# Performance work log

Hardware: AMD Instinct MI355X
Metric: run time of the kernel (lower is better)

The kernel has to match this reference:

```python
import jax, jax.numpy as jnp
import numpy as np

B, D_IN, HID = 8192, 1024, 2048
H_PH, DELTA0 = 64, 7.0
N_EXP, EXP_DIM = 16, 128
VOCAB, N_CLS = 32000, 1000
K_WIN, DECAY, THETA = 20, 0.8, 1.2
N_TOK = 100
ENH = HID + 2 * H_PH  # retrieval-core input dim


def setup_inputs() -> dict:
    key = jax.random.key(0)
    ks = jax.random.split(key, 16)
    s = lambda d: 1.0 / np.sqrt(d)
    return {
        "x": jax.random.normal(ks[0], (B, D_IN), jnp.float32),
        "W_in": jax.random.normal(ks[1], (D_IN, HID), jnp.float32) * s(D_IN),
        "b_in": jnp.zeros((HID,), jnp.float32),
        "Wg": jax.random.normal(ks[2], (ENH, N_EXP), jnp.float32) * s(ENH),
        "bg": jnp.zeros((N_EXP,), jnp.float32),
        "We": jax.random.normal(ks[3], (N_EXP, ENH, EXP_DIM), jnp.float32) * s(ENH),
        "be": jnp.zeros((N_EXP, EXP_DIM), jnp.float32),
        "Wo": jax.random.normal(ks[4], (EXP_DIM, HID), jnp.float32) * s(EXP_DIM),
        "bo": jnp.zeros((HID,), jnp.float32),
        "Wh": jax.random.normal(ks[5], (3, HID, HID), jnp.float32) * s(HID),
        "bh": jnp.zeros((3, HID), jnp.float32),
        "Wcls": jax.random.normal(ks[6], (HID, N_CLS), jnp.float32) * s(HID),
        "bcls": jnp.zeros((N_CLS,), jnp.float32),
    }


def reference(x, W_in, b_in, Wg, bg, We, be, Wo, bo, Wh, bh, Wcls, bcls):
    # input projection
    proj = x @ W_in + b_in                                  # [B, HID]
    # phasor bank on per-sample mean (vmapped oscillator bank)
    t = jnp.mean(proj, axis=-1)                             # [B]
    harm = jnp.arange(1, H_PH + 1, dtype=proj.dtype)        # [H]
    phase = DELTA0 * t[:, None] * harm[None, :]             # [B, H]
    temporal = jnp.concatenate([jnp.sin(phase), jnp.cos(phase)], axis=-1)  # [B, 2H]
    enh = jnp.concatenate([proj, temporal], axis=-1)        # [B, ENH]
    # 16-expert retrieval core: softmax gate, relu experts, dense readout
    gate = jax.nn.softmax(enh @ Wg + bg, axis=-1)           # [B, E]
    expert = jax.nn.relu(jnp.einsum('bd,edk->bek', enh, We) + be)  # [B, E, K]
    combined = jnp.einsum('be,bek->bk', gate, expert)       # [B, K]
    context = combined @ Wo + bo                            # [B, HID]
    # spiking top-k attention over modulo-indexed tokens from sample 0
    tok = jnp.argsort(jnp.abs(context[0]))[-N_TOK:] % VOCAB  # [100] int

    def step(v, ti):
        v = DECAY * v
        v = v.at[ti].add(1.0)
        spk = v > THETA
        return jnp.where(spk, 0.0, v), spk.astype(context.dtype)

    _, spikes = jax.lax.scan(step, jnp.zeros((VOCAB,), context.dtype), tok)
    counts = spikes.sum(axis=0)                             # [VOCAB]
    _, top_idx = jax.lax.top_k(counts, K_WIN)
    gains = jnp.ones((VOCAB,), context.dtype).at[top_idx].add(1.0)
    attended = context * gains[: context.shape[-1]]         # [B, HID]
    # trailing dense MLP
    h = attended
    for i in range(3):
        h = jax.nn.relu(h @ Wh[i] + bh[i])
    return h @ Wcls + bcls                                  # [B, N_CLS]
```

## Files before the change

kernel.cpp:

```cpp
#include <hip/hip_runtime.h>
#include <math.h>


typedef unsigned short u16;
typedef __attribute__((ext_vector_type(8))) short bfrag8;
typedef __attribute__((ext_vector_type(4))) float facc4;

__device__ __forceinline__ u16 f2bf(float f) {
  union { float f; unsigned u; } c; c.f = f;
  unsigned u = c.u;
  return (u16)((u + 0x7fffu + ((u >> 16) & 1u)) >> 16);
}
__device__ __forceinline__ float bf2f(u16 h) {
  union { unsigned u; float f; } c; c.u = ((unsigned)h) << 16;
  return c.f;
}
__device__ __forceinline__ void gload16(const void* g, void* lds) {
  __builtin_amdgcn_global_load_lds(
      (const __attribute__((address_space(1))) unsigned*)g,
      (__attribute__((address_space(3))) unsigned*)lds, 16, 0, 0);
}

#define BARX() do { __builtin_amdgcn_sched_barrier(0); \
  __builtin_amdgcn_s_barrier(); __builtin_amdgcn_sched_barrier(0); } while (0)
#define LGKM0() do { asm volatile("s_waitcnt lgkmcnt(0)" ::: "memory"); \
  __builtin_amdgcn_sched_barrier(0); } while (0)
#define VMWN() do { if constexpr (MFR == 8) \
    asm volatile("s_waitcnt vmcnt(4)" ::: "memory"); \
  else asm volatile("s_waitcnt vmcnt(2)" ::: "memory"); \
  __builtin_amdgcn_sched_barrier(0); } while (0)

#define RDA_(dst, mbase, dbuf) do { \
  char* _b = smem + (dbuf) * DBUF; \
  _Pragma("unroll") for (int mm = 0; mm < MFRH; ++mm) { \
    int _row = wr * (BM / 2) + ((mbase) + mm) * 16 + r15; \
    _Pragma("unroll") for (int ks = 0; ks < 2; ++ks) \
      dst[mm][ks] = *(const bfrag8*)(_b + _row * 128 + \
                                     (((g + ks * 4) ^ (_row & 7)) << 4)); \
  } } while (0)

#define RDB_(dst, nbase, dbuf) do { \
  char* _b = smem + (dbuf) * DBUF + AREG; \
  _Pragma("unroll") for (int nn = 0; nn < 2; ++nn) { \
    int _row = wc * 64 + ((nbase) + nn) * 16 + r15; \
    _Pragma("unroll") for (int ks = 0; ks < 2; ++ks) \
      dst[nn][ks] = *(const bfrag8*)(_b + _row * 128 + \
                                     (((g + ks * 4) ^ (_row & 7)) << 4)); \
  } } while (0)

#define MF_(a, b, mo, no) do { \
  __builtin_amdgcn_s_setprio(1); \
  _Pragma("unroll") for (int mm = 0; mm < MFRH; ++mm) \
  _Pragma("unroll") for (int nn = 0; nn < 2; ++nn) \
  _Pragma("unroll") for (int ks = 0; ks < 2; ++ks) \
    acc[(mo) + mm][(no) + nn] = __builtin_amdgcn_mfma_f32_16x16x32_bf16( \
        a[mm][ks], b[nn][ks], acc[(mo) + mm][(no) + nn], 0, 0, 0); \
  __builtin_amdgcn_s_setprio(0); \
} while (0)

enum { EP_PROJ = 0, EP_EXPERT = 1, EP_CTX = 2, EP_RELU = 3, EP_OUT = 4 };

template<int EP, int MFR>
__global__ __launch_bounds__(512, 2)
void gemm8(const u16* __restrict__ A, const u16* __restrict__ Bt,
           const float* __restrict__ bias, void* __restrict__ Cp,
           const float* __restrict__ gate, float* __restrict__ partials,
           int K, int lda, int ldb, int ldc, int nvalid)
{
  constexpr int MFRH = MFR / 2;
  constexpr int BM = MFR * 32;
  constexpr int AHALF = MFR * 2048;
  constexpr int AREG = MFR * 4096;
  constexpr int DBUF = AREG + 32768;

  extern __shared__ char smem[];
  const int t = threadIdx.x;
  const int lane = t & 63, wid = t >> 6;
  const int wr = wid >> 2, wc = wid & 3;
  const int g = lane >> 4, r15 = lane & 15;

  const int nblk = gridDim.x * gridDim.y;
  const int flat = blockIdx.y * gridDim.x + blockIdx.x;
  const int swz = (flat & 7) * (nblk >> 3) + (flat >> 3);
  const int bx = swz % gridDim.x, by = swz / gridDim.x;

  const long a0 = (long)(by * BM) * lda;
  const long b0 = (long)(bx * 256) * ldb;

  facc4 acc[MFR][4];
#pragma unroll
  for (int m = 0; m < MFR; m++)
#pragma unroll
    for (int n = 0; n < 4; n++) acc[m][n] = (facc4){0.f, 0.f, 0.f, 0.f};

  const int r0 = t >> 3, c0s = t & 7;
  const int csw = ((c0s ^ (r0 & 7)) << 3);

  auto STAGE = [&](int kt, int which, int dbuf) {
    const int half = which & 1;
    if (which < 2) {
      char* ldst = smem + dbuf * DBUF + half * AHALF;
      const u16* gsrc =
          A + a0 + (long)(half * (BM / 2) + r0) * lda + kt * 64 + csw;
      gload16(gsrc, ldst + (t << 4));
      if (MFR == 8) gload16(gsrc + 64L * lda, ldst + ((512 + t) << 4));
    } else {
      char* ldst = smem + dbuf * DBUF + AREG + half * 16384;
      const u16* gsrc =
          Bt + b0 + (long)(half * 128 + r0) * ldb + kt * 64 + csw;
      gload16(gsrc, ldst + (t << 4));
      gload16(gsrc + 64L * ldb, ldst + ((512 + t) << 4));
    }
  };

  const int NT = K >> 6;
  STAGE(0, 0, 0); STAGE(0, 1, 0); STAGE(0, 2, 0); STAGE(0, 3, 0);
  STAGE(1, 0, 1); STAGE(1, 1, 1);
  VMWN(); BARX();

  bfrag8 aE[MFRH][2], aO[MFRH][2], b01[2][2], b23[2][2];

  for (int it = 0; it < (NT >> 1); ++it) {
    const int T = 2 * it;
    const int tp1 = T + 1;
    const int tp2 = (T + 2 < NT) ? T + 2 : NT - 1;
    const int tp3 = (T + 3 < NT) ? T + 3 : NT - 1;
    RDA_(aE, 0, 0); RDB_(b01, 0, 0); STAGE(tp1, 2, 1);
    LGKM0(); MF_(aE, b01, 0, 0); BARX();
    RDA_(aO, MFRH, 0); STAGE(tp1, 3, 1);
    LGKM0(); MF_(aO, b01, MFRH, 0); BARX();
    RDB_(b23, 2, 0); STAGE(tp2, 0, 0); STAGE(tp2, 1, 0);
    LGKM0(); MF_(aO, b23, MFRH, 2); MF_(aE, b23, 0, 2);
    VMWN(); BARX();
    RDA_(aE, 0, 1); RDB_(b01, 0, 1); STAGE(tp2, 2, 0);
    LGKM0(); MF_(aE, b01, 0, 0); BARX();
    RDA_(aO, MFRH, 1); STAGE(tp2, 3, 0);
    LGKM0(); MF_(aO, b01, MFRH, 0); BARX();
    RDB_(b23, 2, 1); STAGE(tp3, 0, 1); STAGE(tp3, 1, 1);
    LGKM0(); MF_(aO, b23, MFRH, 2); MF_(aE, b23, 0, 2);
    VMWN(); BARX();
  }

  asm volatile("s_waitcnt vmcnt(0)" ::: "memory");
  __builtin_amdgcn_sched_barrier(0);
  __builtin_amdgcn_s_barrier();
  __builtin_amdgcn_sched_barrier(0);

  const int rbase = by * BM + wr * (BM / 2);
  const int cbase = bx * 256 + wc * 64;
  float* slab = (float*)(smem + wid * 8704);

  float psum[MFR][4];
  if (EP == EP_PROJ) {
#pragma unroll
    for (int m = 0; m < MFR; m++)
#pragma unroll
      for (int r = 0; r < 4; r++) psum[m][r] = 0.f;
  }

#pragma unroll
  for (int pass = 0; pass < MFRH; ++pass) {
#pragma unroll
    for (int mm = 0; mm < 2; ++mm) {
      const int m = pass * 2 + mm;
#pragma unroll
      for (int n = 0; n < 4; ++n)
#pragma unroll
        for (int r = 0; r < 4; ++r) {
          const int rowp = mm * 16 + g * 4 + r;
          const int grow = rbase + m * 16 + g * 4 + r;
          const int gcol = cbase + n * 16 + r15;
          float val = acc[m][n][r] + bias[gcol];
          if (EP == EP_EXPERT)
            val = fmaxf(val, 0.f) * gate[(long)grow * 16 + (gcol >> 7)];
          if (EP == EP_CTX && gcol < 20) val *= 2.0f;
          if (EP == EP_RELU) val = fmaxf(val, 0.f);
          if (EP == EP_PROJ) psum[m][r] += val;
          slab[rowp * 68 + n * 16 + r15] = val;
        }
    }
#pragma unroll
    for (int rep = 0; rep < 4; ++rep) {
      const int rowp = rep * 8 + (lane >> 3);
      const int cc = (lane & 7) * 8;
      const facc4 v0 = *(const facc4*)&slab[rowp * 68 + cc];
      const facc4 v1 = *(const facc4*)&slab[rowp * 68 + cc + 4];
      const long grow = rbase + pass * 32 + rowp;
      const int gcol0 = cbase + cc;
      if (EP == EP_OUT) {
        float* Cf = (float*)Cp;
        if (gcol0 + 7 < nvalid) {
          *(facc4*)(Cf + grow * ldc + gcol0) = v0;
          *(facc4*)(Cf + grow * ldc + gcol0 + 4) = v1;
        } else {
#pragma unroll
          for (int j = 0; j < 4; ++j)
            if (gcol0 + j < nvalid) Cf[grow * ldc + gcol0 + j] = v0[j];
#pragma unroll
          for (int j = 0; j < 4; ++j)
            if (gcol0 + 4 + j < nvalid) Cf[grow * ldc + gcol0 + 4 + j] = v1[j];
        }
      } else {
        u16 o[8];
        o[0] = f2bf(v0[0]); o[1] = f2bf(v0[1]);
        o[2] = f2bf(v0[2]); o[3] = f2bf(v0[3]);
        o[4] = f2bf(v1[0]); o[5] = f2bf(v1[1]);
        o[6] = f2bf(v1[2]); o[7] = f2bf(v1[3]);
        *(uint4*)((u16*)Cp + grow * ldc + gcol0) = *(const uint4*)o;
      }
    }
  }

  if (EP == EP_PROJ) {
#pragma unroll
    for (int m = 0; m < MFR; m++)
#pragma unroll
      for (int r = 0; r < 4; r++) {
        float p = psum[m][r];
        p += __shfl_xor(p, 1); p += __shfl_xor(p, 2);
        p += __shfl_xor(p, 4); p += __shfl_xor(p, 8);
        if (r15 == 0)
          partials[(long)(rbase + m * 16 + g * 4 + r) * 32 + bx * 4 + wc] = p;
      }
  }
}

__global__ __launch_bounds__(256)
void transpose_conv_k(const float* __restrict__ in, u16* __restrict__ out,
                      int K, int N, int ldout, long in_zstride, int out_zrows)
{
  __shared__ float tile[64][65];
  const int t = threadIdx.x;
  const int n0 = blockIdx.x * 64, k0 = blockIdx.y * 64;
  const float* src = in + (long)blockIdx.z * in_zstride;
  const int rr = t >> 4;
  const int cc = (t & 15) * 4;
#pragma unroll
  for (int j = 0; j < 4; j++) {
    int k = k0 + j * 16 + rr;
    int n = n0 + cc;
    float v0 = 0.f, v1 = 0.f, v2 = 0.f, v3 = 0.f;
    if (n + 3 < N) {
      facc4 v = *(const facc4*)(src + (long)k * N + n);
      v0 = v[0]; v1 = v[1]; v2 = v[2]; v3 = v[3];
    } else {
      if (n < N)     v0 = src[(long)k * N + n];
      if (n + 1 < N) v1 = src[(long)k * N + n + 1];
      if (n + 2 < N) v2 = src[(long)k * N + n + 2];
      if (n + 3 < N) v3 = src[(long)k * N + n + 3];
    }
    float* trow = &tile[j * 16 + rr][cc];
    trow[0] = v0; trow[1] = v1; trow[2] = v2; trow[3] = v3;
  }
  __syncthreads();
  const int n_l = t >> 2;
  const int kc = (t & 3) * 16;
  const int n_gl = n0 + n_l;
  u16 o16[16];
  const bool valid = n_gl < N;
#pragma unroll
  for (int i = 0; i < 16; i++) o16[i] = valid ? f2bf(tile[kc + i][n_l]) : (u16)0;
  long orow = (long)blockIdx.z * out_zrows + n_gl;
  u16* dst = out + orow * (long)ldout + k0 + kc;
  *(uint4*)dst = ((const uint4*)o16)[0];
  *(uint4*)(dst + 8) = ((const uint4*)o16)[1];
}

__global__ __launch_bounds__(256)
void f32_to_bf16_k(const float* __restrict__ in, u16* __restrict__ out)
{
  const long i = ((long)blockIdx.x * 256 + threadIdx.x) * 8;
  facc4 v0 = *(const facc4*)(in + i);
  facc4 v1 = *(const facc4*)(in + i + 4);
  u16 o[8];
  o[0] = f2bf(v0[0]); o[1] = f2bf(v0[1]); o[2] = f2bf(v0[2]); o[3] = f2bf(v0[3]);
  o[4] = f2bf(v1[0]); o[5] = f2bf(v1[1]); o[6] = f2bf(v1[2]); o[7] = f2bf(v1[3]);
  *(uint4*)(out + i) = *(const uint4*)o;
}

__global__ __launch_bounds__(128)
void temporal_k(const float* __restrict__ partials, u16* __restrict__ enh)
{
  __shared__ float tsh;
  const int b = blockIdx.x;
  const int j = threadIdx.x;
  if (j < 32) {
    float p = partials[(long)b * 32 + j];
    p += __shfl_xor(p, 1); p += __shfl_xor(p, 2); p += __shfl_xor(p, 4);
    p += __shfl_xor(p, 8); p += __shfl_xor(p, 16);
    if (j == 0) tsh = p;
  }
  __syncthreads();
  float tmean = tsh * (1.0f / 2048.0f);
  float v;
  if (j < 64) v = sinf(7.0f * tmean * (float)(j + 1));
  else        v = cosf(7.0f * tmean * (float)(j - 63));
  enh[(long)b * 2176 + 2048 + j] = f2bf(v);
}

__global__ __launch_bounds__(64)
void gate2_k(const u16* __restrict__ enh, const u16* __restrict__ Wgt,
             const float* __restrict__ bg, float* __restrict__ gate)
{
  const int lane = threadIdx.x & 63;
  const int g = lane >> 4, r15 = lane & 15;
  const long rowbase = (long)blockIdx.x * 16;

  const u16* arow = enh + (rowbase + r15) * 2176 + g * 8;
  const u16* brow = Wgt + (long)r15 * 2176 + g * 8;

  facc4 acc = (facc4){0.f, 0.f, 0.f, 0.f};
#pragma unroll 4
  for (int kt = 0; kt < 2176; kt += 64) {
    bfrag8 a0 = *(const bfrag8*)(arow + kt);
    bfrag8 b0 = *(const bfrag8*)(brow + kt);
    bfrag8 a1 = *(const bfrag8*)(arow + kt + 32);
    bfrag8 b1 = *(const bfrag8*)(brow + kt + 32);
    acc = __builtin_amdgcn_mfma_f32_16x16x32_bf16(a0, b0, acc, 0, 0, 0);
    acc = __builtin_amdgcn_mfma_f32_16x16x32_bf16(a1, b1, acc, 0, 0, 0);
  }

  const float bb = bg[r15];
#pragma unroll
  for (int r = 0; r < 4; ++r) {
    float v = acc[r] + bb;
    float mx = v;
    mx = fmaxf(mx, __shfl_xor(mx, 1)); mx = fmaxf(mx, __shfl_xor(mx, 2));
    mx = fmaxf(mx, __shfl_xor(mx, 4)); mx = fmaxf(mx, __shfl_xor(mx, 8));
    float ex = expf(v - mx);
    float sum = ex;
    sum += __shfl_xor(sum, 1); sum += __shfl_xor(sum, 2);
    sum += __shfl_xor(sum, 4); sum += __shfl_xor(sum, 8);
    gate[(rowbase + g * 4 + r) * 16 + r15] = ex / sum;
  }
}

__global__ __launch_bounds__(256)
void combine_k(const u16* __restrict__ expw, u16* __restrict__ comb)
{
  const long i = ((long)blockIdx.x * 256 + threadIdx.x) * 8;
  const long b = i >> 7;
  const int k = (int)(i & 127);
  float s[8] = {0.f, 0.f, 0.f, 0.f, 0.f, 0.f, 0.f, 0.f};
#pragma unroll
  for (int e = 0; e < 16; ++e) {
    uint4 v = *(const uint4*)(expw + b * 2048 + e * 128 + k);
    const u16* vp = (const u16*)&v;
#pragma unroll
    for (int j = 0; j < 8; ++j) s[j] += bf2f(vp[j]);
  }
  u16 o[8];
#pragma unroll
  for (int j = 0; j < 8; ++j) o[j] = f2bf(s[j]);
  *(uint4*)(comb + i) = *(const uint4*)o;
}

extern "C" void kernel_launch(void* const* d_in, const int* in_sizes, int n_in,
                              void* d_out, int out_size, void* d_ws,
                              size_t ws_size, hipStream_t stream)
{
  const float* x    = (const float*)d_in[0];
  const float* W_in = (const float*)d_in[1];
  const float* b_in = (const float*)d_in[2];
  const float* Wg   = (const float*)d_in[3];
  const float* bg   = (const float*)d_in[4];
  const float* We   = (const float*)d_in[5];
  const float* be   = (const float*)d_in[6];
  const float* Wo   = (const float*)d_in[7];
  const float* bo   = (const float*)d_in[8];
  const float* Wh   = (const float*)d_in[9];
  const float* bh   = (const float*)d_in[10];
  const float* Wcls = (const float*)d_in[11];
  const float* bcls = (const float*)d_in[12];
  float* out = (float*)d_out;

  char* ws = (char*)d_ws;
  u16* enhb   = (u16*)(ws);
  u16* bufF   = (u16*)(ws + 35651584);
  u16* bufA   = (u16*)(ws + 69206016);
  u16* Wt_o   = (u16*)(ws + 78118912);
  u16* bufW1  = (u16*)(ws + 78643200);
  u16* bufW2  = (u16*)(ws + 87031808);
  u16* comb   = (u16*)(ws + 95420416);
  float* partials = (float*)(ws + 97517568);
  float* gate     = (float*)(ws + 98566144);
  u16* Wt_in  = bufF;
  u16* xb     = bufF + 2097152;
  u16* Wgt    = bufF;
  u16* Wt_e   = bufA;
  u16* Wt_cls = bufA;

  hipFuncSetAttribute((const void*)gemm8<EP_PROJ, 8>,
                      hipFuncAttributeMaxDynamicSharedMemorySize, 131072);
  hipFuncSetAttribute((const void*)gemm8<EP_EXPERT, 8>,
                      hipFuncAttributeMaxDynamicSharedMemorySize, 131072);
  hipFuncSetAttribute((const void*)gemm8<EP_CTX, 8>,
                      hipFuncAttributeMaxDynamicSharedMemorySize, 131072);
  hipFuncSetAttribute((const void*)gemm8<EP_RELU, 8>,
                      hipFuncAttributeMaxDynamicSharedMemorySize, 131072);
  hipFuncSetAttribute((const void*)gemm8<EP_OUT, 4>,
                      hipFuncAttributeMaxDynamicSharedMemorySize, 98304);

  f32_to_bf16_k<<<4096, 256, 0, stream>>>(x, xb);
  transpose_conv_k<<<dim3(32, 16, 1), 256, 0, stream>>>(W_in, Wt_in, 1024, 2048, 1024, 0, 0);
  transpose_conv_k<<<dim3(2, 34, 16), 256, 0, stream>>>(We, Wt_e, 2176, 128, 2176, 2176L * 128L, 128);
  transpose_conv_k<<<dim3(32, 2, 1), 256, 0, stream>>>(Wo, Wt_o, 128, 2048, 128, 0, 0);
  transpose_conv_k<<<dim3(32, 32, 2), 256, 0, stream>>>(Wh, bufW1, 2048, 2048, 2048, 2048L * 2048L, 2048);

  gemm8<EP_PROJ, 8><<<dim3(8, 32), 512, 131072, stream>>>(
      xb, Wt_in, b_in, (void*)enhb, nullptr, partials, 1024, 1024, 1024, 2176, 2048);
  temporal_k<<<8192, 128, 0, stream>>>(partials, enhb);
  transpose_conv_k<<<dim3(1, 34, 1), 256, 0, stream>>>(Wg, Wgt, 2176, 16, 2176, 0, 0);
  gate2_k<<<512, 64, 0, stream>>>(enhb, Wgt, bg, gate);
  gemm8<EP_EXPERT, 8><<<dim3(8, 32), 512, 131072, stream>>>(
      enhb, Wt_e, be, (void*)bufF, gate, nullptr, 2176, 2176, 2176, 2048, 2048);
  transpose_conv_k<<<dim3(16, 32, 1), 256, 0, stream>>>(Wcls, Wt_cls, 2048, 1000, 2048, 0, 0);
  combine_k<<<512, 256, 0, stream>>>(bufF, comb);
  gemm8<EP_CTX, 8><<<dim3(8, 32), 512, 131072, stream>>>(
      comb, Wt_o, bo, (void*)enhb, nullptr, nullptr, 128, 128, 128, 2048, 2048);
  gemm8<EP_RELU, 8><<<dim3(8, 32), 512, 131072, stream>>>(
      enhb, bufW1, bh, (void*)bufF, nullptr, nullptr, 2048, 2048, 2048, 2048, 2048);
  transpose_conv_k<<<dim3(32, 32, 1), 256, 0, stream>>>(Wh + 2L * 2048L * 2048L, bufW1, 2048, 2048, 2048, 0, 0);
  gemm8<EP_RELU, 8><<<dim3(8, 32), 512, 131072, stream>>>(
      bufF, bufW2, bh + 2048, (void*)enhb, nullptr, nullptr, 2048, 2048, 2048, 2048, 2048);
  gemm8<EP_RELU, 8><<<dim3(8, 32), 512, 131072, stream>>>(
      enhb, bufW1, bh + 4096, (void*)bufF, nullptr, nullptr, 2048, 2048, 2048, 2048, 2048);
  gemm8<EP_OUT, 4><<<dim3(4, 64), 512, 98304, stream>>>(
      bufF, Wt_cls, bcls, (void*)out, nullptr, nullptr, 2048, 2048, 2048, 1000, 1000);
}
```

Measured before the change: 377.1 us.

## Switch GEMM inner loop to 32x32x16 MFMA with blocked LDS layout

Replaces the 16x16x32 bf16 MFMA tiles with 32x32x16 MFMA instructions. The LDS staging layout changes from an XOR-swizzled row layout to a blocked layout of 32-row by 8-k chunks, so each lane reads contiguous 16-byte fragments without swizzle math. The epilogue is rewritten for the 16-register accumulator layout, and the projection row-sum reduction moves inside each pass. The aim is fewer MFMA issues and LDS reads per FLOP. The risks are bank conflicts in the unswizzled layout and higher register pressure from the larger accumulators.

```diff
diff --git a/kernel.cpp b/kernel.cpp
--- a/kernel.cpp
+++ b/kernel.cpp
@@ -5,6 +5,7 @@
 typedef unsigned short u16;
 typedef __attribute__((ext_vector_type(8))) short bfrag8;
 typedef __attribute__((ext_vector_type(4))) float facc4;
+typedef __attribute__((ext_vector_type(16))) float facc16;
 
 __device__ __forceinline__ u16 f2bf(float f) {
   union { float f; unsigned u; } c; c.f = f;
@@ -30,31 +31,27 @@
   else asm volatile("s_waitcnt vmcnt(2)" ::: "memory"); \
   __builtin_amdgcn_sched_barrier(0); } while (0)
 
-#define RDA_(dst, mbase, dbuf) do { \
+#define RDA32(dst, mbase, dbuf) do { \
   char* _b = smem + (dbuf) * DBUF; \
-  _Pragma("unroll") for (int mm = 0; mm < MFRH; ++mm) { \
-    int _row = wr * (BM / 2) + ((mbase) + mm) * 16 + r15; \
-    _Pragma("unroll") for (int ks = 0; ks < 2; ++ks) \
-      dst[mm][ks] = *(const bfrag8*)(_b + _row * 128 + \
-                                     (((g + ks * 4) ^ (_row & 7)) << 4)); \
+  _Pragma("unroll") for (int mm = 0; mm < HB; ++mm) { \
+    char* _s = _b + (wr * MBW + (mbase) + mm) * 4096 + l31 * 16 + lh * 512; \
+    _Pragma("unroll") for (int kb = 0; kb < 4; ++kb) \
+      dst[mm][kb] = *(const bfrag8*)(_s + kb * 1024); \
   } } while (0)
 
-#define RDB_(dst, nbase, dbuf) do { \
-  char* _b = smem + (dbuf) * DBUF + AREG; \
-  _Pragma("unroll") for (int nn = 0; nn < 2; ++nn) { \
-    int _row = wc * 64 + ((nbase) + nn) * 16 + r15; \
-    _Pragma("unroll") for (int ks = 0; ks < 2; ++ks) \
-      dst[nn][ks] = *(const bfrag8*)(_b + _row * 128 + \
-                                     (((g + ks * 4) ^ (_row & 7)) << 4)); \
-  } } while (0)
-
-#define MF_(a, b, mo, no) do { \
+#define RDB32(dst, bnh, dbuf) do { \
+  char* _s = smem + (dbuf) * DBUF + AREG + (bnh) * 16384 + wc * 4096 + \
+             l31 * 16 + lh * 512; \
+  _Pragma("unroll") for (int kb = 0; kb < 4; ++kb) \
+    dst[kb] = *(const bfrag8*)(_s + kb * 1024); \
+} while (0)
+
+#define MF32(a, b, mo, nb) do { \
   __builtin_amdgcn_s_setprio(1); \
-  _Pragma("unroll") for (int mm = 0; mm < MFRH; ++mm) \
-  _Pragma("unroll") for (int nn = 0; nn < 2; ++nn) \
-  _Pragma("unroll") for (int ks = 0; ks < 2; ++ks) \
-    acc[(mo) + mm][(no) + nn] = __builtin_amdgcn_mfma_f32_16x16x32_bf16( \
-        a[mm][ks], b[nn][ks], acc[(mo) + mm][(no) + nn], 0, 0, 0); \
+  _Pragma("unroll") for (int kb = 0; kb < 4; ++kb) \
+  _Pragma("unroll") for (int mm = 0; mm < HB; ++mm) \
+    acc[(mo) + mm][nb] = __builtin_amdgcn_mfma_f32_32x32x16_bf16( \
+        a[mm][kb], b[kb], acc[(mo) + mm][nb], 0, 0, 0); \
   __builtin_amdgcn_s_setprio(0); \
 } while (0)
 
@@ -67,7 +64,8 @@
            const float* __restrict__ gate, float* __restrict__ partials,
            int K, int lda, int ldb, int ldc, int nvalid)
 {
-  constexpr int MFRH = MFR / 2;
+  constexpr int MBW = MFR / 2;
+  constexpr int HB = MBW / 2;
   constexpr int BM = MFR * 32;
   constexpr int AHALF = MFR * 2048;
   constexpr int AREG = MFR * 4096;
@@ -77,7 +75,7 @@
   const int t = threadIdx.x;
   const int lane = t & 63, wid = t >> 6;
   const int wr = wid >> 2, wc = wid & 3;
-  const int g = lane >> 4, r15 = lane & 15;
+  const int l31 = lane & 31, lh = lane >> 5;
 
   const int nblk = gridDim.x * gridDim.y;
   const int flat = blockIdx.y * gridDim.x + blockIdx.x;
@@ -87,29 +85,47 @@
   const long a0 = (long)(by * BM) * lda;
   const long b0 = (long)(bx * 256) * ldb;
 
-  facc4 acc[MFR][4];
-#pragma unroll
-  for (int m = 0; m < MFR; m++)
-#pragma unroll
-    for (int n = 0; n < 4; n++) acc[m][n] = (facc4){0.f, 0.f, 0.f, 0.f};
-
-  const int r0 = t >> 3, c0s = t & 7;
-  const int csw = ((c0s ^ (r0 & 7)) << 3);
+  facc16 acc[MBW][2];
+#pragma unroll
+  for (int m = 0; m < MBW; m++)
+#pragma unroll
+    for (int n = 0; n < 2; n++)
+#pragma unroll
+      for (int i = 0; i < 16; i++) acc[m][n][i] = 0.f;
+
+  const int s_kc = (t >> 5) & 7;
+  const int s_r = t & 31;
 
   auto STAGE = [&](int kt, int which, int dbuf) {
     const int half = which & 1;
     if (which < 2) {
       char* ldst = smem + dbuf * DBUF + half * AHALF;
-      const u16* gsrc =
-          A + a0 + (long)(half * (BM / 2) + r0) * lda + kt * 64 + csw;
-      gload16(gsrc, ldst + (t << 4));
-      if (MFR == 8) gload16(gsrc + 64L * lda, ldst + ((512 + t) << 4));
+      {
+        const int mb = t >> 8;
+        const u16* gsrc = A + a0 +
+            (long)(half * (BM / 2) + mb * 32 + s_r) * lda + kt * 64 + s_kc * 8;
+        gload16(gsrc, ldst + (t << 4));
+      }
+      if (MFR == 8) {
+        const int mb = 2 + (t >> 8);
+        const u16* gsrc = A + a0 +
+            (long)(half * (BM / 2) + mb * 32 + s_r) * lda + kt * 64 + s_kc * 8;
+        gload16(gsrc, ldst + ((512 + t) << 4));
+      }
     } else {
       char* ldst = smem + dbuf * DBUF + AREG + half * 16384;
-      const u16* gsrc =
-          Bt + b0 + (long)(half * 128 + r0) * ldb + kt * 64 + csw;
-      gload16(gsrc, ldst + (t << 4));
-      gload16(gsrc + 64L * ldb, ldst + ((512 + t) << 4));
+      {
+        const int s = t >> 8;
+        const u16* gsrc = Bt + b0 +
+            (long)(s * 64 + half * 32 + s_r) * ldb + kt * 64 + s_kc * 8;
+        gload16(gsrc, ldst + (t << 4));
+      }
+      {
+        const int s = 2 + (t >> 8);
+        const u16* gsrc = Bt + b0 +
+            (long)(s * 64 + half * 32 + s_r) * ldb + kt * 64 + s_kc * 8;
+        gload16(gsrc, ldst + ((512 + t) << 4));
+      }
     }
   };
 
@@ -118,26 +134,26 @@
   STAGE(1, 0, 1); STAGE(1, 1, 1);
   VMWN(); BARX();
 
-  bfrag8 aE[MFRH][2], aO[MFRH][2], b01[2][2], b23[2][2];
+  bfrag8 aE[HB][4], aO[HB][4], bn0[4], bn1[4];
 
   for (int it = 0; it < (NT >> 1); ++it) {
     const int T = 2 * it;
     const int tp1 = T + 1;
     const int tp2 = (T + 2 < NT) ? T + 2 : NT - 1;
     const int tp3 = (T + 3 < NT) ? T + 3 : NT - 1;
-    RDA_(aE, 0, 0); RDB_(b01, 0, 0); STAGE(tp1, 2, 1);
-    LGKM0(); MF_(aE, b01, 0, 0); BARX();
-    RDA_(aO, MFRH, 0); STAGE(tp1, 3, 1);
-    LGKM0(); MF_(aO, b01, MFRH, 0); BARX();
-    RDB_(b23, 2, 0); STAGE(tp2, 0, 0); STAGE(tp2, 1, 0);
-    LGKM0(); MF_(aO, b23, MFRH, 2); MF_(aE, b23, 0, 2);
+    RDA32(aE, 0, 0); RDB32(bn0, 0, 0); STAGE(tp1, 2, 1);
+    LGKM0(); MF32(aE, bn0, 0, 0); BARX();
+    RDA32(aO, HB, 0); STAGE(tp1, 3, 1);
+    LGKM0(); MF32(aO, bn0, HB, 0); BARX();
+    RDB32(bn1, 1, 0); STAGE(tp2, 0, 0); STAGE(tp2, 1, 0);
+    LGKM0(); MF32(aO, bn1, HB, 1); MF32(aE, bn1, 0, 1);
     VMWN(); BARX();
-    RDA_(aE, 0, 1); RDB_(b01, 0, 1); STAGE(tp2, 2, 0);
-    LGKM0(); MF_(aE, b01, 0, 0); BARX();
-    RDA_(aO, MFRH, 1); STAGE(tp2, 3, 0);
-    LGKM0(); MF_(aO, b01, MFRH, 0); BARX();
-    RDB_(b23, 2, 1); STAGE(tp3, 0, 1); STAGE(tp3, 1, 1);
-    LGKM0(); MF_(aO, b23, MFRH, 2); MF_(aE, b23, 0, 2);
+    RDA32(aE, 0, 1); RDB32(bn0, 0, 1); STAGE(tp2, 2, 0);
+    LGKM0(); MF32(aE, bn0, 0, 0); BARX();
+    RDA32(aO, HB, 1); STAGE(tp2, 3, 0);
+    LGKM0(); MF32(aO, bn0, HB, 0); BARX();
+    RDB32(bn1, 1, 1); STAGE(tp3, 0, 1); STAGE(tp3, 1, 1);
+    LGKM0(); MF32(aO, bn1, HB, 1); MF32(aE, bn1, 0, 1);
     VMWN(); BARX();
   }
 
@@ -150,34 +166,44 @@
   const int cbase = bx * 256 + wc * 64;
   float* slab = (float*)(smem + wid * 8704);
 
-  float psum[MFR][4];
-  if (EP == EP_PROJ) {
-#pragma unroll
-    for (int m = 0; m < MFR; m++)
-#pragma unroll
-      for (int r = 0; r < 4; r++) psum[m][r] = 0.f;
-  }
-
-#pragma unroll
-  for (int pass = 0; pass < MFRH; ++pass) {
-#pragma unroll
-    for (int mm = 0; mm < 2; ++mm) {
-      const int m = pass * 2 + mm;
-#pragma unroll
-      for (int n = 0; n < 4; ++n)
-#pragma unroll
-        for (int r = 0; r < 4; ++r) {
-          const int rowp = mm * 16 + g * 4 + r;
-          const int grow = rbase + m * 16 + g * 4 + r;
-          const int gcol = cbase + n * 16 + r15;
-          float val = acc[m][n][r] + bias[gcol];
-          if (EP == EP_EXPERT)
-            val = fmaxf(val, 0.f) * gate[(long)grow * 16 + (gcol >> 7)];
-          if (EP == EP_CTX && gcol < 20) val *= 2.0f;
-          if (EP == EP_RELU) val = fmaxf(val, 0.f);
-          if (EP == EP_PROJ) psum[m][r] += val;
-          slab[rowp * 68 + n * 16 + r15] = val;
+  const float bcol0 = bias[cbase + l31];
+  const float bcol1 = bias[cbase + 32 + l31];
+
+#pragma unroll
+  for (int pass = 0; pass < MBW; ++pass) {
+    float pr[16];
+    if (EP == EP_PROJ) {
+#pragma unroll
+      for (int reg = 0; reg < 16; ++reg) pr[reg] = 0.f;
+    }
+#pragma unroll
+    for (int nb = 0; nb < 2; ++nb) {
+      const float bb = nb ? bcol1 : bcol0;
+      const int gcol = cbase + nb * 32 + l31;
+#pragma unroll
+      for (int reg = 0; reg < 16; ++reg) {
+        const int rowp = (reg & 3) + 8 * (reg >> 2) + 4 * lh;
+        const int grow = rbase + pass * 32 + rowp;
+        float val = acc[pass][nb][reg] + bb;
+        if (EP == EP_EXPERT)
+          val = fmaxf(val, 0.f) * gate[(long)grow * 16 + (gcol >> 7)];
+        if (EP == EP_CTX && gcol < 20) val *= 2.0f;
+        if (EP == EP_RELU) val = fmaxf(val, 0.f);
+        if (EP == EP_PROJ) pr[reg] += val;
+        slab[rowp * 68 + nb * 32 + l31] = val;
+      }
+    }
+    if (EP == EP_PROJ) {
+#pragma unroll
+      for (int reg = 0; reg < 16; ++reg) {
+        float p = pr[reg];
+        p += __shfl_xor(p, 1); p += __shfl_xor(p, 2);
+        p += __shfl_xor(p, 4); p += __shfl_xor(p, 8); p += __shfl_xor(p, 16);
+        if (l31 == 0) {
+          const int rowp = (reg & 3) + 8 * (reg >> 2) + 4 * lh;
+          partials[(long)(rbase + pass * 32 + rowp) * 32 + bx * 4 + wc] = p;
         }
+      }
     }
 #pragma unroll
     for (int rep = 0; rep < 4; ++rep) {
@@ -209,19 +235,6 @@
         *(uint4*)((u16*)Cp + grow * ldc + gcol0) = *(const uint4*)o;
       }
     }
-  }
-
-  if (EP == EP_PROJ) {
-#pragma unroll
-    for (int m = 0; m < MFR; m++)
-#pragma unroll
-      for (int r = 0; r < 4; r++) {
-        float p = psum[m][r];
-        p += __shfl_xor(p, 1); p += __shfl_xor(p, 2);
-        p += __shfl_xor(p, 4); p += __shfl_xor(p, 8);
-        if (r15 == 0)
-          partials[(long)(rbase + m * 16 + g * 4 + r) * 32 + bx * 4 + wc] = p;
-      }
   }
 }
 
```

Result: slower. 475.0 us (+26.0%).
